# Performance work log

Hardware: AMD Instinct MI355X
Metric: run time of the kernel (lower is better)

## Reference

```python
import jax, jax.numpy as jnp
import numpy as np

# config constants (from init_kwargs)
DT = 1.0
TAU_J = 10.0
TAU_M = 20.0
KAPPA_J = 0.25
A_GEN = 1.0
A_DISC = 1.0
THRESH = 0.4
X_DECAY = 20.0  # trace decay constant: x += -x/20 + spikes

B = 8192
LS = [1024, 512, 512, 256]


def setup_inputs() -> dict:
    key = jax.random.key(0)
    ks = jax.random.split(key, 24)
    inp = {}
    inp['x_input'] = (jax.random.uniform(ks[0], (B, LS[0])) < 0.2).astype(jnp.float32)
    inp['y_target'] = (jax.random.uniform(ks[1], (B, LS[3])) < 0.2).astype(jnp.float32)
    # hidden-layer states (layers 1 and 2); layer 0 / last are clamped
    inp['j1'] = jax.random.normal(ks[2], (B, LS[1])) * 0.1
    inp['v1'] = jax.random.normal(ks[3], (B, LS[1])) * 0.1
    inp['s1'] = (jax.random.uniform(ks[4], (B, LS[1])) < 0.2).astype(jnp.float32)
    inp['x1'] = jax.random.uniform(ks[5], (B, LS[1])) * 2.0
    inp['j2'] = jax.random.normal(ks[6], (B, LS[2])) * 0.1
    inp['v2'] = jax.random.normal(ks[7], (B, LS[2])) * 0.1
    inp['s2'] = (jax.random.uniform(ks[8], (B, LS[2])) < 0.2).astype(jnp.float32)
    inp['x2'] = jax.random.uniform(ks[9], (B, LS[2])) * 2.0
    # weights (torch.rand * 0.01)
    inp['W0'] = jax.random.uniform(ks[10], (LS[0], LS[1])) * 0.01
    inp['W1'] = jax.random.uniform(ks[11], (LS[1], LS[2])) * 0.01
    inp['W2'] = jax.random.uniform(ks[12], (LS[2], LS[3])) * 0.01
    inp['V0'] = jax.random.uniform(ks[13], (LS[1], LS[0])) * 0.01
    inp['V1'] = jax.random.uniform(ks[14], (LS[2], LS[1])) * 0.01
    inp['V2'] = jax.random.uniform(ks[15], (LS[3], LS[2])) * 0.01
    inp['Eg0'] = jax.random.uniform(ks[16], (LS[1], LS[0])) * 0.01
    inp['Eg1'] = jax.random.uniform(ks[17], (LS[2], LS[1])) * 0.01
    inp['Eg2'] = jax.random.uniform(ks[18], (LS[3], LS[2])) * 0.01
    inp['Ed0'] = jax.random.uniform(ks[19], (LS[0], LS[1])) * 0.01
    inp['Ed1'] = jax.random.uniform(ks[20], (LS[1], LS[2])) * 0.01
    inp['Ed2'] = jax.random.uniform(ks[21], (LS[2], LS[3])) * 0.01
    return inp


def _lif_update(j, v, x, total_input):
    # Eq 19-24: leaky current integrator -> leaky membrane -> threshold -> reset -> trace
    j = j + (DT / TAU_J) * (-KAPPA_J * j + total_input)
    v = v + (DT / TAU_M) * (-v + j)  # uses updated j, as in the torch code
    spikes = (v > THRESH).astype(v.dtype)
    v = v * (1.0 - spikes)  # hard reset
    x = x + (-x / X_DECAY + spikes)  # spike trace
    return j, v, spikes, x


def reference(x_input, y_target, j1, v1, s1, x1, j2, v2, s2, x2,
              W0, W1, W2, V0, V1, V2, Eg0, Eg1, Eg2, Ed0, Ed1, Ed2):
    # --- phase 1: error neurons (all layers, using current spikes) ---
    # layer 0 clamped: x0 = x_input, s0 = x_input; layer 3 clamped: x3 = s3 = y_target
    e_gen0 = A_GEN * (x_input - s1 @ W0.T)       # [B, 1024]
    e_gen1 = A_GEN * (x1 - s2 @ W1.T)            # [B, 512]
    e_gen2 = A_GEN * (x2 - y_target @ W2.T)      # [B, 512]
    e_disc1 = A_DISC * (x1 - x_input @ V0.T)     # [B, 512]
    e_disc2 = A_DISC * (x2 - s1 @ V1.T)          # [B, 512]
    e_disc3 = A_DISC * (y_target - s2 @ V2.T)    # [B, 256]

    # --- phase 2: value-neuron updates (hidden layers 1 and 2 only) ---
    total1 = -(e_gen1 + e_disc1) + e_gen0 @ Eg0.T + e_disc2 @ Ed1.T
    total2 = -(e_gen2 + e_disc2) + e_gen1 @ Eg1.T + e_disc3 @ Ed2.T

    j1n, v1n, s1n, x1n = _lif_update(j1, v1, x1, total1)
    j2n, v2n, s2n, x2n = _lif_update(j2, v2, x2, total2)

    return jnp.concatenate([j1n, v1n, x1n, s1n, j2n, v2n, x2n, s2n], axis=-1)  # [B, 4096]
```

## Files before the change

### kernel.cpp

```cpp
#include <hip/hip_runtime.h>
#include <stdint.h>
#include <stddef.h>

typedef unsigned short u16;
typedef __attribute__((ext_vector_type(8))) short short8;
typedef __attribute__((ext_vector_type(4))) float f32x4;

#define DEVI __device__ __forceinline__

DEVI u16 f2bf(float f) {
  union { float f; unsigned u; } c; c.f = f;
  unsigned r = c.u + 0x7fff + ((c.u >> 16) & 1);
  return (u16)(r >> 16);
}

DEVI short8 pack8(f32x4 a, f32x4 b) {
  short8 v;
#pragma unroll
  for (int i = 0; i < 4; i++) { v[i] = (short)f2bf(a[i]); v[i + 4] = (short)f2bf(b[i]); }
  return v;
}

typedef __attribute__((address_space(1))) const void global_cvoid;
typedef __attribute__((address_space(3))) void lds_void;


DEVI void mfma_phase(const u16* As, const u16* Bs, f32x4 acc[4][4])
{
  const int lane = threadIdx.x & 63;
  const int w    = threadIdx.x >> 6;
  const int l16  = lane & 15, lq = lane >> 4;
  const int wm   = (w >> 1) * 64, wn = (w & 1) * 64;
#pragma unroll
  for (int kc = 0; kc < 2; kc++) {
    short8 afr[4], bfr[4];
#pragma unroll
    for (int rt = 0; rt < 4; rt++) {
      int m  = wm + rt * 16 + l16;
      int gr = (kc * 4 + lq) ^ (m & 7);
      afr[rt] = *(const short8*)(As + m * 64 + gr * 8);
    }
#pragma unroll
    for (int ct = 0; ct < 4; ct++) {
      int n  = wn + ct * 16 + l16;
      int gr = (kc * 4 + lq) ^ (n & 7);
      bfr[ct] = *(const short8*)(Bs + n * 64 + gr * 8);
    }
#pragma unroll
    for (int rt = 0; rt < 4; rt++)
#pragma unroll
      for (int ct = 0; ct < 4; ct++)
        acc[rt][ct] = __builtin_amdgcn_mfma_f32_16x16x32_bf16(afr[rt], bfr[ct], acc[rt][ct], 0, 0, 0);
  }
}

DEVI void mfma_phase32(const u16* As, const u16* Bs, f32x4 acc[2][2])
{
  const int lane = threadIdx.x & 63;
  const int w    = threadIdx.x >> 6;
  const int l16  = lane & 15, lq = lane >> 4;
  const int wm   = (w >> 1) * 32, wn = (w & 1) * 32;
#pragma unroll
  for (int kc = 0; kc < 2; kc++) {
    short8 afr[2], bfr[2];
#pragma unroll
    for (int rt = 0; rt < 2; rt++) {
      int m  = wm + rt * 16 + l16;
      int gr = (kc * 4 + lq) ^ (m & 7);
      afr[rt] = *(const short8*)(As + m * 64 + gr * 8);
    }
#pragma unroll
    for (int ct = 0; ct < 2; ct++) {
      int n  = wn + ct * 16 + l16;
      int gr = (kc * 4 + lq) ^ (n & 7);
      bfr[ct] = *(const short8*)(Bs + n * 64 + gr * 8);
    }
#pragma unroll
    for (int rt = 0; rt < 2; rt++)
#pragma unroll
      for (int ct = 0; ct < 2; ct++)
        acc[rt][ct] = __builtin_amdgcn_mfma_f32_16x16x32_bf16(afr[rt], bfr[ct], acc[rt][ct], 0, 0, 0);
  }
}

DEVI void zero_acc(f32x4 acc[4][4]) {
  f32x4 z = {0.f, 0.f, 0.f, 0.f};
#pragma unroll
  for (int a = 0; a < 4; a++)
#pragma unroll
    for (int b = 0; b < 4; b++) acc[a][b] = z;
}

DEVI void zero_acc22(f32x4 acc[2][2]) {
  f32x4 z = {0.f, 0.f, 0.f, 0.f};
#pragma unroll
  for (int a = 0; a < 2; a++)
#pragma unroll
    for (int b = 0; b < 2; b++) acc[a][b] = z;
}

struct Params {
  const float *x_input, *y_target, *j1, *v1, *s1, *x1, *j2, *v2, *s2, *x2;
  const float *W0, *W1, *W2, *V0, *V1, *V2, *Eg0, *Eg1, *Ed1, *Ed2;
};


template <int RR>
DEVI void stage_async(const u16* gbase, int ldr, int k0, u16* lds)
{
  const int t = threadIdx.x;
  const int lane = t & 63, w = t >> 6;
#pragma unroll
  for (int tt = 0; tt < RR; tt++) {
    int rowbase = w * (RR * 8) + tt * 8;
    int row = rowbase + (lane >> 3);
    int gsw = (lane & 7) ^ (row & 7);
    __builtin_amdgcn_global_load_lds(
        (global_cvoid*)(gbase + (size_t)row * ldr + k0 + gsw * 8),
        (lds_void*)(lds + rowbase * 64), 16, 0, 0);
  }
}

DEVI void gemm_term64(const u16* A, const u16* B, int K,
                      u16* As, u16* Bs, f32x4 acc[2][2])
{
  for (int k0 = 0; k0 < K; k0 += 64) {
    stage_async<2>(A, K, k0, As);
    stage_async<2>(B, K, k0, Bs);
    __syncthreads();
    mfma_phase32(As, Bs, acc);
    __syncthreads();
  }
}

struct PJob { const float *s0, *s1; u16* dst; int start; };
struct TJob { const float* in; u16* out; int J, tbase; };
struct PrepArgs { PJob jb[14]; TJob tj[4]; };

__global__ __launch_bounds__(256) void k_prep(PrepArgs A)
{
  __shared__ u16 T[32][33];
  int b = blockIdx.x;
  int t = threadIdx.x;
  if (b < 14464) {
    int ji = 0;
#pragma unroll
    for (int i = 1; i < 14; i++)
      if (b >= A.jb[i].start) ji = i;
    PJob pj = A.jb[ji];
    size_t e0 = ((size_t)(b - pj.start) * 256 + t) * 8;
    const float* s0 = pj.s0 + e0;
    f32x4 a  = *(const f32x4*)s0;
    f32x4 b4 = *(const f32x4*)(s0 + 4);
    if (pj.s1) {
      const float* s1 = pj.s1 + e0;
      a  = a  + *(const f32x4*)s1;
      b4 = b4 + *(const f32x4*)(s1 + 4);
    }
    *(short8*)(pj.dst + e0) = pack8(a, b4);
    return;
  }
  int b2 = b - 14464;
  int ji = 0;
#pragma unroll
  for (int i = 1; i < 4; i++)
    if (b2 >= A.tj[i].tbase) ji = i;
  TJob jb = A.tj[ji];
  int local = b2 - jb.tbase;
  int tm = local >> 4;
  int tk = local & 15;
  int tx = t & 31, ty = t >> 5;
#pragma unroll
  for (int i = 0; i < 4; i++) {
    int r = ty + i * 8;
    T[r][tx] = f2bf(jb.in[(size_t)(tm * 32 + r) * 512 + tk * 32 + tx]);
  }
  __syncthreads();
#pragma unroll
  for (int i = 0; i < 4; i++) {
    int r = ty + i * 8;
    jb.out[(size_t)(tk * 32 + r) * jb.J + tm * 32 + tx] = T[tx][r];
  }
}

struct BW2Args {
  const u16 *Eg0b, *W0tb, *Ed1b, *V1tb, *Eg1b, *W1tb, *Ed2b, *V2tb;
  u16 *Bw1b, *Bw2b;
};

__global__ __launch_bounds__(256) void k_bw2(BW2Args A)
{
  __shared__ u16 As[64 * 64];
  __shared__ u16 Bs[64 * 64];
  int b   = blockIdx.x;
  int mat = b >> 6, loc = b & 63;
  int bmw = loc >> 3, bnw = loc & 7;

  f32x4 acc[2][2];
  zero_acc22(acc);
  u16* dst;
  if (mat == 0) {
    gemm_term64(A.Eg0b + (size_t)bmw * 64 * 1024, A.W0tb + (size_t)bnw * 64 * 1024, 1024, As, Bs, acc);
    gemm_term64(A.Ed1b + (size_t)bmw * 64 * 512,  A.V1tb + (size_t)bnw * 64 * 512,   512, As, Bs, acc);
    dst = A.Bw1b;
  } else {
    gemm_term64(A.Eg1b + (size_t)bmw * 64 * 512,  A.W1tb + (size_t)bnw * 64 * 512,   512, As, Bs, acc);
    gemm_term64(A.Ed2b + (size_t)bmw * 64 * 256,  A.V2tb + (size_t)bnw * 64 * 256,   256, As, Bs, acc);
    dst = A.Bw2b;
  }
  const int lane = threadIdx.x & 63;
  const int w    = threadIdx.x >> 6;
  const int l16  = lane & 15, lq = lane >> 4;
  const int wm   = (w >> 1) * 32, wn = (w & 1) * 32;
#pragma unroll
  for (int rt = 0; rt < 2; rt++)
#pragma unroll
    for (int ct = 0; ct < 2; ct++)
#pragma unroll
      for (int i = 0; i < 4; i++) {
        int rl = wm + rt * 16 + lq * 4 + i;
        int cl = wn + ct * 16 + l16;
        dst[(size_t)(bmw * 64 + rl) * 512 + bnw * 64 + cl] = f2bf(-acc[rt][ct][i]);
      }
}

struct MJobF {
  const u16* A[4]; const u16* B[4]; int K[4];
  const float *jin, *vin, *xin;
  int obase;
};
struct MArgsF { MJobF j[2]; };

__global__ __launch_bounds__(256, 8) void k_main_fast(MArgsF P, float* __restrict__ out)
{
  __shared__ u16 As[64 * 64];
  __shared__ u16 Bs[64 * 64];
  int bid   = blockIdx.x;
  int job   = bid >> 10;
  int local = bid & 1023;
  int bm = local & 127, bn = local >> 7;
  MJobF jb = P.j[job];

  switch (((bid >> 8) ^ bid) & 3) {
    case 1: __builtin_amdgcn_s_sleep(8); break;
    case 2: __builtin_amdgcn_s_sleep(8); __builtin_amdgcn_s_sleep(8); break;
    case 3: __builtin_amdgcn_s_sleep(8); __builtin_amdgcn_s_sleep(8);
            __builtin_amdgcn_s_sleep(8); break;
    default: break;
  }

  f32x4 acc[2][2];
  zero_acc22(acc);
#pragma unroll
  for (int p = 0; p < 4; p++)
    gemm_term64(jb.A[p] + (size_t)bm * 64 * jb.K[p],
                jb.B[p] + (size_t)bn * 64 * jb.K[p], jb.K[p], As, Bs, acc);

  const int lane = threadIdx.x & 63;
  const int w    = threadIdx.x >> 6;
  const int l16  = lane & 15, lq = lane >> 4;
  const int wm   = (w >> 1) * 32, wn = (w & 1) * 32;

#pragma unroll
  for (int rt = 0; rt < 2; rt++)
#pragma unroll
    for (int ct = 0; ct < 2; ct++)
#pragma unroll
      for (int i = 0; i < 4; i++) {
        int row    = bm * 64 + wm + rt * 16 + lq * 4 + i;
        int col    = bn * 64 + wn + ct * 16 + l16;
        size_t idx = (size_t)row * 512 + col;
        float xf = jb.xin[idx];
        float total = acc[rt][ct][i] - 2.0f * xf;
        float jf = jb.jin[idx];
        float vf = jb.vin[idx];
        jf = jf + 0.1f * (-0.25f * jf + total);
        vf = vf + 0.05f * (-vf + jf);
        float sf = (vf > 0.4f) ? 1.0f : 0.0f;
        vf = vf * (1.0f - sf);
        xf = xf + (-xf / 20.0f + sf);
        size_t ob = (size_t)row * 4096 + jb.obase + col;
        out[ob]        = jf;
        out[ob + 512]  = vf;
        out[ob + 1024] = xf;
        out[ob + 1536] = sf;
      }
}


DEVI void stage_A_fb(const float* A, int ldr, int k0, u16* dst)
{
  const int t = threadIdx.x;
  const int g = t & 7, rb = t >> 3;
#pragma unroll
  for (int p = 0; p < 4; p++) {
    int row = p * 32 + rb;
    const float* src = A + (size_t)row * ldr + k0 + g * 8;
    f32x4 a = *(const f32x4*)src;
    f32x4 b = *(const f32x4*)(src + 4);
    *(short8*)(dst + row * 64 + (g ^ (row & 7)) * 8) = pack8(a, b);
  }
}

DEVI void nn_term_fb(const float* A, const float* B, int K, u16* As, u16* Bs, f32x4 acc[4][4])
{
  const int t  = threadIdx.x;
  const int ks = t >> 4, ng = t & 15;
  for (int k0 = 0; k0 < K; k0 += 64) {
    stage_A_fb(A, K, k0, As);
#pragma unroll
    for (int i = 0; i < 4; i++) {
      int kloc = i * 16 + ks;
      const float* src = B + (size_t)(k0 + kloc) * 512 + ng * 8;
      f32x4 a = *(const f32x4*)src;
      f32x4 b = *(const f32x4*)(src + 4);
#pragma unroll
      for (int e = 0; e < 8; e++) {
        int nloc = ng * 8 + e;
        float val = (e < 4) ? a[e] : b[e - 4];
        Bs[nloc * 64 + ((kloc >> 3) ^ (nloc & 7)) * 8 + (kloc & 7)] = f2bf(val);
      }
    }
    __syncthreads();
    mfma_phase(As, Bs, acc);
    __syncthreads();
  }
}

template <int MODE>
DEVI void gemm_term_fb(const float* A, const float* B0, const float* B1, int K,
                       u16* As, u16* Bs, f32x4 acc[4][4])
{
  const int t = threadIdx.x;
  const int g = t & 7, rb = t >> 3;
  for (int k0 = 0; k0 < K; k0 += 64) {
    stage_A_fb(A, K, k0, As);
#pragma unroll
    for (int p = 0; p < 4; p++) {
      int row = p * 32 + rb;
      const float* src;
      if (MODE == 2) src = B0 + (size_t)row * 4096 + (k0 >> 7) * 512 + (k0 & 127) + g * 8;
      else           src = B0 + (size_t)row * K + k0 + g * 8;
      f32x4 a = *(const f32x4*)src;
      f32x4 b = *(const f32x4*)(src + 4);
      if (MODE == 1) {
        const float* s2 = B1 + (size_t)row * K + k0 + g * 8;
        a = a + *(const f32x4*)s2;
        b = b + *(const f32x4*)(s2 + 4);
      }
      *(short8*)(Bs + row * 64 + (g ^ (row & 7)) * 8) = pack8(a, b);
    }
    __syncthreads();
    mfma_phase(As, Bs, acc);
    __syncthreads();
  }
}

__global__ __launch_bounds__(256) void k_bw_fb(Params P, float* __restrict__ out)
{
  __shared__ u16 As[128 * 64];
  __shared__ u16 Bs[128 * 64];
  int b   = blockIdx.x;
  int mat = b >> 4, loc = b & 15;
  int bmw = loc >> 2, bnw = loc & 3;

  f32x4 acc[4][4];
  zero_acc(acc);
  int obase;
  if (mat == 0) {
    nn_term_fb(P.Eg0 + (size_t)bmw * 128 * 1024, P.W0 + bnw * 128, 1024, As, Bs, acc);
    nn_term_fb(P.Ed1 + (size_t)bmw * 128 * 512,  P.V1 + bnw * 128,  512, As, Bs, acc);
    obase = 0;
  } else {
    nn_term_fb(P.Eg1 + (size_t)bmw * 128 * 512,  P.W1 + bnw * 128,  512, As, Bs, acc);
    nn_term_fb(P.Ed2 + (size_t)bmw * 128 * 256,  P.V2 + bnw * 128,  256, As, Bs, acc);
    obase = 2048;
  }
  const int lane = threadIdx.x & 63;
  const int w    = threadIdx.x >> 6;
  const int l16  = lane & 15, lq = lane >> 4;
  const int wm   = (w >> 1) * 64, wn = (w & 1) * 64;
#pragma unroll
  for (int rt = 0; rt < 4; rt++)
#pragma unroll
    for (int ct = 0; ct < 4; ct++)
#pragma unroll
      for (int i = 0; i < 4; i++) {
        int rl = wm + rt * 16 + lq * 4 + i;
        int cl = wn + ct * 16 + l16;
        out[(size_t)rl * 4096 + obase + bmw * 128 + bnw * 512 + cl] = -acc[rt][ct][i];
      }
}

__global__ __launch_bounds__(256) void k_main_fb(Params P, float* __restrict__ out, int fix)
{
  __shared__ u16 As[128 * 64];
  __shared__ u16 Bs[128 * 64];
  int job, bm, bn;
  if (fix) {
    job = blockIdx.x >> 2; bn = blockIdx.x & 3; bm = 0;
  } else {
    job = blockIdx.x >> 8;
    int local = blockIdx.x & 255;
    bm = local & 63; bn = local >> 6;
    if (bm == 0) return;
  }

  f32x4 acc[4][4];
  zero_acc(acc);
  const float *jin, *vin, *xin;
  int obase;
  size_t am = (size_t)bm * 128;

  if (job == 0) {
    gemm_term_fb<0>(P.s2      + am * 512,  P.W1  + (size_t)bn * 128 * 512,  nullptr, 512,  As, Bs, acc);
    gemm_term_fb<1>(P.x_input + am * 1024, P.V0  + (size_t)bn * 128 * 1024,
                    P.Eg0 + (size_t)bn * 128 * 1024, 1024, As, Bs, acc);
    gemm_term_fb<0>(P.x2      + am * 512,  P.Ed1 + (size_t)bn * 128 * 512,  nullptr, 512,  As, Bs, acc);
    gemm_term_fb<2>(P.s1      + am * 512,  out + 0 + bn * 128,              nullptr, 512,  As, Bs, acc);
    jin = P.j1; vin = P.v1; xin = P.x1; obase = 0;
  } else {
    gemm_term_fb<1>(P.y_target + am * 256, P.W2  + (size_t)bn * 128 * 256,
                    P.Ed2 + (size_t)bn * 128 * 256, 256, As, Bs, acc);
    gemm_term_fb<0>(P.s1      + am * 512,  P.V1  + (size_t)bn * 128 * 512,  nullptr, 512,  As, Bs, acc);
    gemm_term_fb<0>(P.x1      + am * 512,  P.Eg1 + (size_t)bn * 128 * 512,  nullptr, 512,  As, Bs, acc);
    gemm_term_fb<2>(P.s2      + am * 512,  out + 2048 + bn * 128,           nullptr, 512,  As, Bs, acc);
    jin = P.j2; vin = P.v2; xin = P.x2; obase = 2048;
  }

  const int lane = threadIdx.x & 63;
  const int w    = threadIdx.x >> 6;
  const int l16  = lane & 15, lq = lane >> 4;
  const int wm   = (w >> 1) * 64, wn = (w & 1) * 64;

#pragma unroll
  for (int rt = 0; rt < 4; rt++)
#pragma unroll
    for (int ct = 0; ct < 4; ct++)
#pragma unroll
      for (int i = 0; i < 4; i++) {
        int row    = bm * 128 + wm + rt * 16 + lq * 4 + i;
        int col    = bn * 128 + wn + ct * 16 + l16;
        size_t idx = (size_t)row * 512 + col;
        float xf = xin[idx];
        float total = acc[rt][ct][i] - 2.0f * xf;
        float jf = jin[idx];
        float vf = vin[idx];
        jf = jf + 0.1f * (-0.25f * jf + total);
        vf = vf + 0.05f * (-vf + jf);
        float sf = (vf > 0.4f) ? 1.0f : 0.0f;
        vf = vf * (1.0f - sf);
        xf = xf + (-xf / 20.0f + sf);
        size_t ob = (size_t)row * 4096 + obase + col;
        out[ob]        = jf;
        out[ob + 512]  = vf;
        out[ob + 1024] = xf;
        out[ob + 1536] = sf;
      }
}

extern "C" void kernel_launch(void* const* d_in, const int* in_sizes, int n_in,
                              void* d_out, int out_size, void* d_ws, size_t ws_size,
                              hipStream_t stream)
{
  Params P;
  P.x_input  = (const float*)d_in[0];
  P.y_target = (const float*)d_in[1];
  P.j1 = (const float*)d_in[2];
  P.v1 = (const float*)d_in[3];
  P.s1 = (const float*)d_in[4];
  P.x1 = (const float*)d_in[5];
  P.j2 = (const float*)d_in[6];
  P.v2 = (const float*)d_in[7];
  P.s2 = (const float*)d_in[8];
  P.x2 = (const float*)d_in[9];
  P.W0 = (const float*)d_in[10];
  P.W1 = (const float*)d_in[11];
  P.W2 = (const float*)d_in[12];
  P.V0 = (const float*)d_in[13];
  P.V1 = (const float*)d_in[14];
  P.V2 = (const float*)d_in[15];
  P.Eg0 = (const float*)d_in[16];
  P.Eg1 = (const float*)d_in[17];
  P.Ed1 = (const float*)d_in[20];
  P.Ed2 = (const float*)d_in[21];
  (void)in_sizes; (void)n_in; (void)out_size;

  float* out = (float*)d_out;

  if (ws_size >= 62652416) {
    char* ws = (char*)d_ws;
    u16* xin_b = (u16*)(ws + 0);
    u16* y_b   = (u16*)(ws + 16777216);
    u16* s1_b  = (u16*)(ws + 20971520);
    u16* x1_b  = (u16*)(ws + 29360128);
    u16* s2_b  = (u16*)(ws + 37748736);
    u16* x2_b  = (u16*)(ws + 46137344);
    u16* W1_b  = (u16*)(ws + 54525952);
    u16* P1_b  = (u16*)(ws + 55050240);
    u16* Ed1_b = (u16*)(ws + 56098816);
    u16* V1_b  = (u16*)(ws + 56623104);
    u16* Eg1_b = (u16*)(ws + 57147392);
    u16* P2_b  = (u16*)(ws + 57671680);
    u16* Bw1_b = (u16*)(ws + 57933824);
    u16* Bw2_b = (u16*)(ws + 58458112);
    u16* W0t_b = (u16*)(ws + 58982400);
    u16* V1t_b = (u16*)(ws + 60030976);
    u16* W1t_b = (u16*)(ws + 60555264);
    u16* V2t_b = (u16*)(ws + 61079552);
    u16* Eg0_b = (u16*)(ws + 61341696);
    u16* Ed2_b = (u16*)(ws + 62390272);

    PrepArgs pa;
    pa.jb[0]  = { P.x_input,  nullptr, xin_b,     0 };
    pa.jb[1]  = { P.y_target, nullptr, y_b,    4096 };
    pa.jb[2]  = { P.s1,       nullptr, s1_b,   5120 };
    pa.jb[3]  = { P.x1,       nullptr, x1_b,   7168 };
    pa.jb[4]  = { P.s2,       nullptr, s2_b,   9216 };
    pa.jb[5]  = { P.x2,       nullptr, x2_b,  11264 };
    pa.jb[6]  = { P.W1,       nullptr, W1_b,  13312 };
    pa.jb[7]  = { P.V0,       P.Eg0,   P1_b,  13440 };
    pa.jb[8]  = { P.Ed1,      nullptr, Ed1_b, 13696 };
    pa.jb[9]  = { P.V1,       nullptr, V1_b,  13824 };
    pa.jb[10] = { P.Eg1,      nullptr, Eg1_b, 13952 };
    pa.jb[11] = { P.W2,       P.Ed2,   P2_b,  14080 };
    pa.jb[12] = { P.Eg0,      nullptr, Eg0_b, 14144 };
    pa.jb[13] = { P.Ed2,      nullptr, Ed2_b, 14400 };
    pa.tj[0]  = { P.W0, W0t_b, 1024,    0 };
    pa.tj[1]  = { P.V1, V1t_b,  512,  512 };
    pa.tj[2]  = { P.W1, W1t_b,  512,  768 };
    pa.tj[3]  = { P.V2, V2t_b,  256, 1024 };
    k_prep<<<dim3(15616), dim3(256), 0, stream>>>(pa);

    BW2Args ba;
    ba.Eg0b = Eg0_b; ba.W0tb = W0t_b; ba.Ed1b = Ed1_b; ba.V1tb = V1t_b;
    ba.Eg1b = Eg1_b; ba.W1tb = W1t_b; ba.Ed2b = Ed2_b; ba.V2tb = V2t_b;
    ba.Bw1b = Bw1_b; ba.Bw2b = Bw2_b;
    k_bw2<<<dim3(128), dim3(256), 0, stream>>>(ba);

    MArgsF ma;
    ma.j[0].A[0] = s2_b;  ma.j[0].B[0] = W1_b;  ma.j[0].K[0] = 512;
    ma.j[0].A[1] = xin_b; ma.j[0].B[1] = P1_b;  ma.j[0].K[1] = 1024;
    ma.j[0].A[2] = x2_b;  ma.j[0].B[2] = Ed1_b; ma.j[0].K[2] = 512;
    ma.j[0].A[3] = s1_b;  ma.j[0].B[3] = Bw1_b; ma.j[0].K[3] = 512;
    ma.j[0].jin = P.j1; ma.j[0].vin = P.v1; ma.j[0].xin = P.x1; ma.j[0].obase = 0;
    ma.j[1].A[0] = y_b;   ma.j[1].B[0] = P2_b;  ma.j[1].K[0] = 256;
    ma.j[1].A[1] = s1_b;  ma.j[1].B[1] = V1_b;  ma.j[1].K[1] = 512;
    ma.j[1].A[2] = x1_b;  ma.j[1].B[2] = Eg1_b; ma.j[1].K[2] = 512;
    ma.j[1].A[3] = s2_b;  ma.j[1].B[3] = Bw2_b; ma.j[1].K[3] = 512;
    ma.j[1].jin = P.j2; ma.j[1].vin = P.v2; ma.j[1].xin = P.x2; ma.j[1].obase = 2048;
    k_main_fast<<<dim3(2048), dim3(256), 0, stream>>>(ma, out);
  } else {
    k_bw_fb<<<dim3(32), dim3(256), 0, stream>>>(P, out);
    k_main_fb<<<dim3(512), dim3(256), 0, stream>>>(P, out, 0);
    k_main_fb<<<dim3(8), dim3(256), 0, stream>>>(P, out, 1);
  }
}
```

Before: 412.1 us.

## Load MFMA fragments directly from global memory and widen main-kernel tile to 64x128

The main fused GEMM+LIF kernel no longer stages A/B tiles through LDS with async loads and barriers. Each wave now reads its bf16 fragments straight from global memory into registers. The block tile widens from 64x64 to 64x128, which halves the grid and lowers the occupancy hint to 4. The aim is to drop LDS round-trips and __syncthreads stalls, relying on L1/L2 caching for cross-wave reuse. The risks are uncoalesced strided global loads, since each lane reads 16 bytes from a different row, and less explicit data reuse.

```diff
diff --git a/kernel.cpp b/kernel.cpp
--- a/kernel.cpp
+++ b/kernel.cpp
@@ -97,6 +97,14 @@
   for (int a = 0; a < 2; a++)
 #pragma unroll
     for (int b = 0; b < 2; b++) acc[a][b] = z;
+}
+
+DEVI void zero_acc24(f32x4 acc[2][4]) {
+  f32x4 z = {0.f, 0.f, 0.f, 0.f};
+#pragma unroll
+  for (int a = 0; a < 2; a++)
+#pragma unroll
+    for (int b = 0; b < 4; b++) acc[a][b] = z;
 }
 
 struct Params {
@@ -130,6 +138,37 @@
     __syncthreads();
     mfma_phase32(As, Bs, acc);
     __syncthreads();
+  }
+}
+
+DEVI void gemm_term_direct(const u16* A, const u16* B, int K, f32x4 acc[2][4])
+{
+  const int lane = threadIdx.x & 63;
+  const int w    = threadIdx.x >> 6;
+  const int l16  = lane & 15, lq = lane >> 4;
+  const int wm   = (w >> 1) * 32, wn = (w & 1) * 64;
+  const u16* pa0 = A + (size_t)(wm +  0 + l16) * K + lq * 8;
+  const u16* pa1 = A + (size_t)(wm + 16 + l16) * K + lq * 8;
+  const u16* pb0 = B + (size_t)(wn +  0 + l16) * K + lq * 8;
+  const u16* pb1 = B + (size_t)(wn + 16 + l16) * K + lq * 8;
+  const u16* pb2 = B + (size_t)(wn + 32 + l16) * K + lq * 8;
+  const u16* pb3 = B + (size_t)(wn + 48 + l16) * K + lq * 8;
+  const int nk = K >> 5;
+#pragma unroll 4
+  for (int kc = 0; kc < nk; kc++) {
+    int ko = kc * 32;
+    short8 afr[2], bfr[4];
+    afr[0] = *(const short8*)(pa0 + ko);
+    afr[1] = *(const short8*)(pa1 + ko);
+    bfr[0] = *(const short8*)(pb0 + ko);
+    bfr[1] = *(const short8*)(pb1 + ko);
+    bfr[2] = *(const short8*)(pb2 + ko);
+    bfr[3] = *(const short8*)(pb3 + ko);
+#pragma unroll
+    for (int rt = 0; rt < 2; rt++)
+#pragma unroll
+      for (int ct = 0; ct < 4; ct++)
+        acc[rt][ct] = __builtin_amdgcn_mfma_f32_16x16x32_bf16(afr[rt], bfr[ct], acc[rt][ct], 0, 0, 0);
   }
 }
 
@@ -231,13 +270,11 @@
 };
 struct MArgsF { MJobF j[2]; };
 
-__global__ __launch_bounds__(256, 8) void k_main_fast(MArgsF P, float* __restrict__ out)
-{
-  __shared__ u16 As[64 * 64];
-  __shared__ u16 Bs[64 * 64];
+__global__ __launch_bounds__(256, 4) void k_main_fast(MArgsF P, float* __restrict__ out)
+{
   int bid   = blockIdx.x;
-  int job   = bid >> 10;
-  int local = bid & 1023;
+  int job   = bid >> 9;
+  int local = bid & 511;
   int bm = local & 127, bn = local >> 7;
   MJobF jb = P.j[job];
 
@@ -249,26 +286,26 @@
     default: break;
   }
 
-  f32x4 acc[2][2];
-  zero_acc22(acc);
+  f32x4 acc[2][4];
+  zero_acc24(acc);
 #pragma unroll
   for (int p = 0; p < 4; p++)
-    gemm_term64(jb.A[p] + (size_t)bm * 64 * jb.K[p],
-                jb.B[p] + (size_t)bn * 64 * jb.K[p], jb.K[p], As, Bs, acc);
-
-  const int lane = threadIdx.x & 63;
-  const int w    = threadIdx.x >> 6;
-  const int l16  = lane & 15, lq = lane >> 4;
-  const int wm   = (w >> 1) * 32, wn = (w & 1) * 32;
+    gemm_term_direct(jb.A[p] + (size_t)bm * 64 * jb.K[p],
+                     jb.B[p] + (size_t)bn * 128 * jb.K[p], jb.K[p], acc);
+
+  const int lane = threadIdx.x & 63;
+  const int w    = threadIdx.x >> 6;
+  const int l16  = lane & 15, lq = lane >> 4;
+  const int wm   = (w >> 1) * 32, wn = (w & 1) * 64;
 
 #pragma unroll
   for (int rt = 0; rt < 2; rt++)
 #pragma unroll
-    for (int ct = 0; ct < 2; ct++)
+    for (int ct = 0; ct < 4; ct++)
 #pragma unroll
       for (int i = 0; i < 4; i++) {
         int row    = bm * 64 + wm + rt * 16 + lq * 4 + i;
-        int col    = bn * 64 + wn + ct * 16 + l16;
+        int col    = bn * 128 + wn + ct * 16 + l16;
         size_t idx = (size_t)row * 512 + col;
         float xf = jb.xin[idx];
         float total = acc[rt][ct][i] - 2.0f * xf;
@@ -549,7 +586,7 @@
     ma.j[1].A[2] = x1_b;  ma.j[1].B[2] = Eg1_b; ma.j[1].K[2] = 512;
     ma.j[1].A[3] = s2_b;  ma.j[1].B[3] = Bw2_b; ma.j[1].K[3] = 512;
     ma.j[1].jin = P.j2; ma.j[1].vin = P.v2; ma.j[1].xin = P.x2; ma.j[1].obase = 2048;
-    k_main_fast<<<dim3(2048), dim3(256), 0, stream>>>(ma, out);
+    k_main_fast<<<dim3(1024), dim3(256), 0, stream>>>(ma, out);
   } else {
     k_bw_fb<<<dim3(32), dim3(256), 0, stream>>>(P, out);
     k_main_fb<<<dim3(512), dim3(256), 0, stream>>>(P, out, 0);
```

New measurement: 538.0 us. 1.31x slower.
